# Kernel optimization log

Hardware: AMD Instinct MI355X
Metric: run time of the kernel (lower is better)

The kernel has to match this reference:

```python
import jax, jax.numpy as jnp
import numpy as np
import math

B, T, D = 4, 2048, 1024
NHEAD = 16
HEAD_DIM = D // NHEAD
MAX_REL = 16  # max_relative_position default


def setup_inputs() -> dict:
    key = jax.random.key(0)
    ks = jax.random.split(key, 10)
    s = 1.0 / math.sqrt(D)
    inp = {
        "x": jax.random.normal(ks[0], (B, T, D), dtype=jnp.float32),
        "Wq": jax.random.normal(ks[1], (D, D), dtype=jnp.float32) * s,
        "bq": jnp.zeros((D,), dtype=jnp.float32),
        "Wk": jax.random.normal(ks[2], (D, D), dtype=jnp.float32) * s,
        "bk": jnp.zeros((D,), dtype=jnp.float32),
        "Wv": jax.random.normal(ks[3], (D, D), dtype=jnp.float32) * s,
        "bv": jnp.zeros((D,), dtype=jnp.float32),
        "rel_bias": jax.random.normal(ks[4], (2 * MAX_REL - 1, NHEAD), dtype=jnp.float32) * 0.02,
        "Wo": jax.random.normal(ks[5], (D, D), dtype=jnp.float32) * s,
        "bo": jnp.zeros((D,), dtype=jnp.float32),
    }
    return inp


def _relative_bias(rel_bias, seq_len):
    # distance matrix clamped to [-(MAX_REL-1), MAX_REL-1], shifted to index table
    r = jnp.arange(seq_len)
    dist = jnp.clip(r[None, :] - r[:, None], -MAX_REL + 1, MAX_REL - 1) + MAX_REL - 1
    # gather: [T, T, H] -> [H, T, T]
    return jnp.transpose(rel_bias[dist], (2, 0, 1))


def reference(x, Wq, bq, Wk, bk, Wv, bv, rel_bias, Wo, bo):
    Bdim, Tdim, Ddim = x.shape
    # torch Linear: x @ W.T + b
    Q = x @ Wq.T + bq
    K = x @ Wk.T + bk
    V = x @ Wv.T + bv
    # [B, H, T, hd]
    Q = Q.reshape(Bdim, Tdim, NHEAD, HEAD_DIM).transpose(0, 2, 1, 3)
    K = K.reshape(Bdim, Tdim, NHEAD, HEAD_DIM).transpose(0, 2, 1, 3)
    V = V.reshape(Bdim, Tdim, NHEAD, HEAD_DIM).transpose(0, 2, 1, 3)
    scores = jnp.einsum("bhqd,bhkd->bhqk", Q, K) / math.sqrt(HEAD_DIM)
    scores = scores + _relative_bias(rel_bias, Tdim)[None]  # [1,H,T,T]
    attn = jax.nn.softmax(scores, axis=-1)
    out = jnp.einsum("bhqk,bhkd->bhqd", attn, V)
    out = out.transpose(0, 2, 1, 3).reshape(Bdim, Tdim, Ddim)
    return out @ Wo.T + bo
```

## Files before the change

### kernel.cpp

```cpp
#include <hip/hip_runtime.h>
#include <stdint.h>
#include <math.h>

typedef unsigned short u16;
typedef __bf16 bf16x8 __attribute__((ext_vector_type(8)));
typedef float f32x4 __attribute__((ext_vector_type(4)));
typedef float f32x16 __attribute__((ext_vector_type(16)));
typedef unsigned short u16x8 __attribute__((ext_vector_type(8)));
typedef unsigned short u16x4 __attribute__((ext_vector_type(4)));

#define BATCH 4
#define SEQT 2048
#define DMODEL 1024
#define NHEAD 16
#define HDIM 64
#define LOG2E 1.44269504f

#define LDS_GLD16(gp, lp)                                                     \
  __builtin_amdgcn_global_load_lds(                                           \
      (const __attribute__((address_space(1))) void*)(gp),                    \
      (__attribute__((address_space(3))) void*)(lp), 16, 0, 0)

static __device__ __forceinline__ u16 f2bf(float f) {
  union { float f; uint32_t u; } c; c.f = f;
  uint32_t u = c.u;
  return (u16)((u + 0x7fffu + ((u >> 16) & 1u)) >> 16);
}
static __device__ __forceinline__ u16 f2bf_fast(float f) {
  union { float f; uint32_t u; } c; c.f = f;
  return (u16)((c.u + 0x8000u) >> 16);
}
static __device__ __forceinline__ uint32_t pkbf(float a, float b) {
  union { float f; uint32_t u; } ca, cb; ca.f = a; cb.f = b;
  return __builtin_amdgcn_perm(cb.u + 0x8000u, ca.u + 0x8000u, 0x07060302u);
}
static __device__ __forceinline__ bf16x8 mk_bf8(uint32_t x0, uint32_t x1,
                                                uint32_t x2, uint32_t x3) {
  union { uint32_t u[4]; bf16x8 v; } t;
  t.u[0] = x0; t.u[1] = x1; t.u[2] = x2; t.u[3] = x3;
  return t.v;
}

__global__ __launch_bounds__(256) void k_convert_all(
    const float* __restrict__ x, const float* __restrict__ Wq,
    const float* __restrict__ Wk, const float* __restrict__ Wv,
    const float* __restrict__ Wo, u16* __restrict__ xbf,
    u16* __restrict__ Wqkv, u16* __restrict__ Wob) {
  const int NX4 = 2097152, NW4 = 262144;
  int i = blockIdx.x * 256 + threadIdx.x;
  const float* s; u16* d; int js, jd;
  if (i < NX4) {
    s = x; d = xbf; js = jd = i;
  } else if (i < NX4 + 3 * NW4) {
    int j = i - NX4;
    int w = j >> 18;
    s = (w == 0) ? Wq : (w == 1) ? Wk : Wv;
    js = j & (NW4 - 1);
    d = Wqkv; jd = j;
  } else {
    s = Wo; d = Wob; js = jd = i - NX4 - 3 * NW4;
  }
  float4 v = ((const float4*)s)[js];
  u16x4 o = {f2bf(v.x), f2bf(v.y), f2bf(v.z), f2bf(v.w)};
  ((u16x4*)d)[jd] = o;
}

__global__ __launch_bounds__(256) void k_gemm_qk(
    const u16* __restrict__ A, const u16* __restrict__ Bqk,
    const float* __restrict__ bq_, const float* __restrict__ bk_,
    u16* __restrict__ dq, u16* __restrict__ dk) {
  __shared__ u16 As[128 * 64];
  __shared__ u16 Bs[128 * 64];

  const int tid = threadIdx.x;
  const int wave = tid >> 6, lane = tid & 63;
  const int quad = lane >> 4, l16 = lane & 15;
  const int wm = wave & 1, wn = wave >> 1;
  const int m0 = blockIdx.x * 128, n0 = blockIdx.y * 128;
  const int lrow = lane >> 3, lcol = (lane & 7) * 8;

  f32x4 acc[4][4] = {};

  for (int kt = 0; kt < 1024; kt += 64) {
    __syncthreads();
    for (int c = 0; c < 4; ++c) {
      int rr = (wave * 4 + c) * 8 + lrow;
      LDS_GLD16(A + (size_t)(m0 + rr) * 1024 + kt + lcol,
                &As[(wave * 4 + c) * 512]);
      LDS_GLD16(Bqk + (size_t)(n0 + rr) * 1024 + kt + lcol,
                &Bs[(wave * 4 + c) * 512]);
    }
    __syncthreads();
    for (int kh = 0; kh < 2; ++kh) {
      bf16x8 af[4], bfr[4];
      for (int mt = 0; mt < 4; ++mt)
        af[mt] = *(const bf16x8*)&As[(wm * 64 + mt * 16 + l16) * 64 + kh * 32 +
                                     quad * 8];
      for (int nt = 0; nt < 4; ++nt)
        bfr[nt] = *(const bf16x8*)&Bs[(wn * 64 + nt * 16 + l16) * 64 + kh * 32 +
                                      quad * 8];
      for (int mt = 0; mt < 4; ++mt)
        for (int nt = 0; nt < 4; ++nt)
          acc[mt][nt] = __builtin_amdgcn_mfma_f32_16x16x32_bf16(
              af[mt], bfr[nt], acc[mt][nt], 0, 0, 0);
    }
  }

  u16* dst = (n0 < 1024) ? dq : dk;
  const float* bias = (n0 < 1024) ? bq_ : bk_;
  for (int mt = 0; mt < 4; ++mt)
    for (int nt = 0; nt < 4; ++nt) {
      int nn = (n0 + wn * 64 + nt * 16 + l16) & 1023;
      float bv = bias[nn];
      int h = nn >> 6, hd = nn & 63;
      for (int r = 0; r < 4; ++r) {
        int m = m0 + wm * 64 + mt * 16 + quad * 4 + r;
        int b = m >> 11, t = m & 2047;
        dst[(((size_t)b * NHEAD + h) * SEQT + t) * HDIM + hd] =
            f2bf_fast(acc[mt][nt][r] + bv);
      }
    }
}

__global__ __launch_bounds__(256) void k_gemm_vt(const u16* __restrict__ A,
                                                 const u16* __restrict__ Bx,
                                                 const float* __restrict__ bv_,
                                                 u16* __restrict__ Vt) {
  __shared__ u16 As[128 * 64];
  __shared__ u16 Bs[128 * 64];
  __shared__ float biasS[128];

  const int tid = threadIdx.x;
  const int wave = tid >> 6, lane = tid & 63;
  const int quad = lane >> 4, l16 = lane & 15;
  const int wm = wave & 1, wn = wave >> 1;
  const int m0 = blockIdx.x * 128, n0 = blockIdx.y * 128;
  const int lrow = lane >> 3, lcol = (lane & 7) * 8;

  if (tid < 128) biasS[tid] = bv_[m0 + tid];

  f32x4 acc[4][4] = {};

  for (int kt = 0; kt < 1024; kt += 64) {
    __syncthreads();
    for (int c = 0; c < 4; ++c) {
      int rr = (wave * 4 + c) * 8 + lrow;
      LDS_GLD16(A + (size_t)(m0 + rr) * 1024 + kt + lcol,
                &As[(wave * 4 + c) * 512]);
      LDS_GLD16(Bx + (size_t)(n0 + rr) * 1024 + kt + lcol,
                &Bs[(wave * 4 + c) * 512]);
    }
    __syncthreads();
    for (int kh = 0; kh < 2; ++kh) {
      bf16x8 af[4], bfr[4];
      for (int mt = 0; mt < 4; ++mt)
        af[mt] = *(const bf16x8*)&As[(wm * 64 + mt * 16 + l16) * 64 + kh * 32 +
                                     quad * 8];
      for (int nt = 0; nt < 4; ++nt)
        bfr[nt] = *(const bf16x8*)&Bs[(wn * 64 + nt * 16 + l16) * 64 + kh * 32 +
                                      quad * 8];
      for (int mt = 0; mt < 4; ++mt)
        for (int nt = 0; nt < 4; ++nt)
          acc[mt][nt] = __builtin_amdgcn_mfma_f32_16x16x32_bf16(
              af[mt], bfr[nt], acc[mt][nt], 0, 0, 0);
    }
  }

  for (int mt = 0; mt < 4; ++mt)
    for (int nt = 0; nt < 4; ++nt) {
      int n = n0 + wn * 64 + nt * 16 + l16;
      int b = n >> 11, t = n & 2047;
      for (int r = 0; r < 4; ++r) {
        int m = m0 + wm * 64 + mt * 16 + quad * 4 + r;
        float v = acc[mt][nt][r] + biasS[m - m0];
        Vt[((size_t)(b * NHEAD + (m >> 6)) * HDIM + (m & 63)) * SEQT + t] =
            f2bf_fast(v);
      }
    }
}

__global__ __launch_bounds__(256) void k_gemm_proj(const u16* __restrict__ A,
                                                   const u16* __restrict__ Bm,
                                                   const float* __restrict__ bias,
                                                   float* __restrict__ out) {
  __shared__ u16 As[128 * 64];
  __shared__ u16 Bs[128 * 64];

  const int tid = threadIdx.x;
  const int wave = tid >> 6, lane = tid & 63;
  const int quad = lane >> 4, l16 = lane & 15;
  const int wm = wave & 1, wn = wave >> 1;
  const int m0 = blockIdx.x * 128, n0 = blockIdx.y * 128;
  const int lrow = lane >> 3, lcol = (lane & 7) * 8;

  f32x4 acc[4][4] = {};

  for (int kt = 0; kt < 1024; kt += 64) {
    __syncthreads();
    for (int c = 0; c < 4; ++c) {
      int rr = (wave * 4 + c) * 8 + lrow;
      LDS_GLD16(A + (size_t)(m0 + rr) * 1024 + kt + lcol,
                &As[(wave * 4 + c) * 512]);
      LDS_GLD16(Bm + (size_t)(n0 + rr) * 1024 + kt + lcol,
                &Bs[(wave * 4 + c) * 512]);
    }
    __syncthreads();
    for (int kh = 0; kh < 2; ++kh) {
      bf16x8 af[4], bfr[4];
      for (int mt = 0; mt < 4; ++mt)
        af[mt] = *(const bf16x8*)&As[(wm * 64 + mt * 16 + l16) * 64 + kh * 32 +
                                     quad * 8];
      for (int nt = 0; nt < 4; ++nt)
        bfr[nt] = *(const bf16x8*)&Bs[(wn * 64 + nt * 16 + l16) * 64 + kh * 32 +
                                      quad * 8];
      for (int mt = 0; mt < 4; ++mt)
        for (int nt = 0; nt < 4; ++nt)
          acc[mt][nt] = __builtin_amdgcn_mfma_f32_16x16x32_bf16(
              af[mt], bfr[nt], acc[mt][nt], 0, 0, 0);
    }
  }

  for (int mt = 0; mt < 4; ++mt)
    for (int nt = 0; nt < 4; ++nt) {
      int n = n0 + wn * 64 + nt * 16 + l16;
      float bv = bias[n];
      for (int r = 0; r < 4; ++r) {
        int m = m0 + wm * 64 + mt * 16 + quad * 4 + r;
        out[(size_t)m * 1024 + n] = acc[mt][nt][r] + bv;
      }
    }
}

__global__ __launch_bounds__(256, 4) void k_attn(const u16* __restrict__ Qb,
                                                 const u16* __restrict__ Kb,
                                                 const u16* __restrict__ Vt,
                                                 const float* __restrict__ relb,
                                                 u16* __restrict__ Obf) {
  __shared__ u16 Ks[64 * 64];
  __shared__ u16 VTs[64 * 64];
  __shared__ float biasL[32];

  const int tid = threadIdx.x;
  const int wave = tid >> 6, lane = tid & 63;
  const int l32 = lane & 31, hi = lane >> 5;
  const int qt = blockIdx.x;
  const int bh = blockIdx.y;
  const int h = bh & (NHEAD - 1);
  const size_t base = (size_t)bh * SEQT * HDIM;
  const int qa = qt * 128 + wave * 32;

  if (tid < 31) biasL[tid] = relb[tid * NHEAD + h] * LOG2E;
  const float bLo = relb[0 * NHEAD + h] * LOG2E;
  const float bHi = relb[30 * NHEAD + h] * LOG2E;
  const float CL = 0.125f * LOG2E;

  bf16x8 bq[4];
  {
    const u16* qp = Qb + base + (size_t)(qa + l32) * HDIM + hi * 8;
    for (int ds = 0; ds < 4; ++ds) bq[ds] = *(const bf16x8*)(qp + ds * 16);
  }

  f32x16 Oacc[2] = {};
  float ls = 0.f;

  const int rl = lane >> 3, gb = lane & 7;
  const int row0 = wave * 8 + rl, row1 = row0 + 32;
  const u16* kgp0 = Kb + base + (size_t)row0 * HDIM + ((gb ^ (row0 & 7)) << 3);
  const u16* kgp1 = Kb + base + (size_t)row1 * HDIM + ((gb ^ (row1 & 7)) << 3);
  const u16* vgp0 = Vt + base + (size_t)row0 * SEQT + ((gb ^ (row0 & 7)) << 3);
  const u16* vgp1 = Vt + base + (size_t)row1 * SEQT + ((gb ^ (row1 & 7)) << 3);
  u16* ksl0 = &Ks[wave * 512 + lane * 8];
  u16* ksl1 = ksl0 + 2048;
  u16* vsl0 = &VTs[wave * 512 + lane * 8];
  u16* vsl1 = vsl0 + 2048;

  for (int kt2 = 0; kt2 < 32; ++kt2) {
    const int k0 = kt2 * 64;
    __syncthreads();
    LDS_GLD16(kgp0 + (size_t)k0 * HDIM, ksl0);
    LDS_GLD16(kgp1 + (size_t)k0 * HDIM, ksl1);
    LDS_GLD16(vgp0 + k0, vsl0);
    LDS_GLD16(vgp1 + k0, vsl1);
    __syncthreads();

    for (int kgrp = 0; kgrp < 2; ++kgrp) {
      const int kb = k0 + kgrp * 32;
      f32x16 c = {};
      for (int ds = 0; ds < 4; ++ds) {
        const int key = kgrp * 32 + l32;
        bf16x8 ak = *(const bf16x8*)&Ks[key * 64 +
                                        (((ds * 2 + hi) ^ (key & 7)) << 3)];
        c = __builtin_amdgcn_mfma_f32_32x32x16_bf16(ak, bq[ds], c, 0, 0, 0);
      }

      const int dmin = kb - (qa + 31);
      if (dmin >= 15 || kb + 31 - qa <= -15) {
        const float ub = (dmin >= 15) ? bHi : bLo;
        for (int i = 0; i < 16; ++i)
          c[i] = __builtin_amdgcn_exp2f(fmaf(c[i], CL, ub));
      } else {
        const int dbase = kb + 4 * hi - (qa + l32);
        for (int i = 0; i < 16; ++i) {
          int d = dbase + (i & 3) + 8 * (i >> 2);
          d = d < -15 ? -15 : (d > 15 ? 15 : d);
          c[i] = __builtin_amdgcn_exp2f(fmaf(c[i], CL, biasL[d + 15]));
        }
      }
      {
        float s0 = (c[0] + c[1]) + (c[2] + c[3]);
        float s1 = (c[4] + c[5]) + (c[6] + c[7]);
        float s2 = (c[8] + c[9]) + (c[10] + c[11]);
        float s3 = (c[12] + c[13]) + (c[14] + c[15]);
        ls += (s0 + s1) + (s2 + s3);
      }

      uint32_t p[8];
      for (int i = 0; i < 8; ++i) p[i] = pkbf(c[2 * i], c[2 * i + 1]);

      for (int ks = 0; ks < 2; ++ks) {
        bf16x8 bp = mk_bf8(p[ks * 4 + 0], p[ks * 4 + 1], p[ks * 4 + 2],
                           p[ks * 4 + 3]);
        const int blk = kgrp * 4 + ks * 2;
        for (int dg = 0; dg < 2; ++dg) {
          const int d = dg * 32 + l32;
          const int sw = d & 7;
          uint2 a0 = *(const uint2*)&VTs[d * 64 + ((blk ^ sw) << 3) + 4 * hi];
          uint2 a1 =
              *(const uint2*)&VTs[d * 64 + (((blk + 1) ^ sw) << 3) + 4 * hi];
          bf16x8 av = mk_bf8(a0.x, a0.y, a1.x, a1.y);
          Oacc[dg] = __builtin_amdgcn_mfma_f32_32x32x16_bf16(av, bp, Oacc[dg],
                                                             0, 0, 0);
        }
      }
    }
  }

  ls += __shfl_xor(ls, 32, 64);
  const float rinv = 1.0f / ls;

  const int b = bh >> 4;
  const int t = qa + l32;
  u16* op = Obf + ((size_t)(b * SEQT + t)) * DMODEL + h * HDIM;
  for (int dg = 0; dg < 2; ++dg)
    for (int a = 0; a < 4; ++a) {
      uint2 w;
      w.x = pkbf(Oacc[dg][4 * a + 0] * rinv, Oacc[dg][4 * a + 1] * rinv);
      w.y = pkbf(Oacc[dg][4 * a + 2] * rinv, Oacc[dg][4 * a + 3] * rinv);
      *(uint2*)(op + dg * 32 + 8 * a + 4 * hi) = w;
    }
}

extern "C" void kernel_launch(void* const* d_in, const int* in_sizes, int n_in,
                              void* d_out, int out_size, void* d_ws,
                              size_t ws_size, hipStream_t stream) {
  const float* x = (const float*)d_in[0];
  const float* Wq = (const float*)d_in[1];
  const float* bq = (const float*)d_in[2];
  const float* Wk = (const float*)d_in[3];
  const float* bk = (const float*)d_in[4];
  const float* Wv = (const float*)d_in[5];
  const float* bv = (const float*)d_in[6];
  const float* relb = (const float*)d_in[7];
  const float* Wo = (const float*)d_in[8];
  const float* bo = (const float*)d_in[9];
  float* out = (float*)d_out;

  char* ws = (char*)d_ws;
  const size_t SZ_X = (size_t)BATCH * SEQT * DMODEL * 2;
  const size_t SZ_W = (size_t)DMODEL * DMODEL * 2;
  u16* xbf = (u16*)(ws);
  u16* Wqb = (u16*)(ws + SZ_X);
  u16* Wvb = (u16*)(ws + SZ_X + 2 * SZ_W);
  u16* Wob = (u16*)(ws + SZ_X + 3 * SZ_W);
  u16* Qb = (u16*)(ws + SZ_X + 4 * SZ_W);
  u16* Kb = (u16*)(ws + 2 * SZ_X + 4 * SZ_W);
  u16* Vt = (u16*)(ws + 3 * SZ_X + 4 * SZ_W);
  u16* Obf = (u16*)(ws + 4 * SZ_X + 4 * SZ_W);

  k_convert_all<<<12288, 256, 0, stream>>>(x, Wq, Wk, Wv, Wo, xbf, Wqb, Wob);
  k_gemm_qk<<<dim3(64, 16), 256, 0, stream>>>(xbf, Wqb, bq, bk, Qb, Kb);
  k_gemm_vt<<<dim3(8, 64), 256, 0, stream>>>(Wvb, xbf, bv, Vt);
  k_attn<<<dim3(16, 64), 256, 0, stream>>>(Qb, Kb, Vt, relb, Obf);
  k_gemm_proj<<<dim3(64, 8), 256, 0, stream>>>(Obf, Wob, bo, out);
}
```

Measured before the change: 316.2 us.

## Merge QK and V-transpose GEMMs into one launch and permute Vt for vector LDS reads

```diff
diff --git a/kernel.cpp b/kernel.cpp
--- a/kernel.cpp
+++ b/kernel.cpp
@@ -5,6 +5,7 @@
 typedef unsigned short u16;
 typedef __bf16 bf16x8 __attribute__((ext_vector_type(8)));
 typedef float f32x4 __attribute__((ext_vector_type(4)));
+typedef float f32x2 __attribute__((ext_vector_type(2)));
 typedef float f32x16 __attribute__((ext_vector_type(16)));
 typedef unsigned short u16x8 __attribute__((ext_vector_type(8)));
 typedef unsigned short u16x4 __attribute__((ext_vector_type(4)));
@@ -65,18 +66,29 @@
   ((u16x4*)d)[jd] = o;
 }
 
-__global__ __launch_bounds__(256) void k_gemm_qk(
-    const u16* __restrict__ A, const u16* __restrict__ Bqk,
-    const float* __restrict__ bq_, const float* __restrict__ bk_,
-    u16* __restrict__ dq, u16* __restrict__ dk) {
+__global__ __launch_bounds__(256) void k_gemm_qkvt(
+    const u16* __restrict__ xbf, const u16* __restrict__ Wqk,
+    const u16* __restrict__ Wv, const float* __restrict__ bq_,
+    const float* __restrict__ bk_, const float* __restrict__ bv_,
+    u16* __restrict__ dq, u16* __restrict__ dk, u16* __restrict__ Vt) {
   __shared__ u16 As[128 * 64];
   __shared__ u16 Bs[128 * 64];
+
+  const int bid = blockIdx.x;
+  const bool isQK = bid < 1024;
+  const u16 *Ap, *Bp;
+  int m0, n0;
+  if (isQK) {
+    m0 = (bid & 63) * 128; n0 = (bid >> 6) * 128; Ap = xbf; Bp = Wqk;
+  } else {
+    int j = bid - 1024;
+    m0 = (j & 7) * 128; n0 = (j >> 3) * 128; Ap = Wv; Bp = xbf;
+  }
 
   const int tid = threadIdx.x;
   const int wave = tid >> 6, lane = tid & 63;
   const int quad = lane >> 4, l16 = lane & 15;
   const int wm = wave & 1, wn = wave >> 1;
-  const int m0 = blockIdx.x * 128, n0 = blockIdx.y * 128;
   const int lrow = lane >> 3, lcol = (lane & 7) * 8;
 
   f32x4 acc[4][4] = {};
@@ -85,9 +97,9 @@
     __syncthreads();
     for (int c = 0; c < 4; ++c) {
       int rr = (wave * 4 + c) * 8 + lrow;
-      LDS_GLD16(A + (size_t)(m0 + rr) * 1024 + kt + lcol,
+      LDS_GLD16(Ap + (size_t)(m0 + rr) * 1024 + kt + lcol,
                 &As[(wave * 4 + c) * 512]);
-      LDS_GLD16(Bqk + (size_t)(n0 + rr) * 1024 + kt + lcol,
+      LDS_GLD16(Bp + (size_t)(n0 + rr) * 1024 + kt + lcol,
                 &Bs[(wave * 4 + c) * 512]);
     }
     __syncthreads();
@@ -106,29 +118,43 @@
     }
   }
 
-  u16* dst = (n0 < 1024) ? dq : dk;
-  const float* bias = (n0 < 1024) ? bq_ : bk_;
-  for (int mt = 0; mt < 4; ++mt)
-    for (int nt = 0; nt < 4; ++nt) {
-      int nn = (n0 + wn * 64 + nt * 16 + l16) & 1023;
-      float bv = bias[nn];
-      int h = nn >> 6, hd = nn & 63;
-      for (int r = 0; r < 4; ++r) {
-        int m = m0 + wm * 64 + mt * 16 + quad * 4 + r;
-        int b = m >> 11, t = m & 2047;
-        dst[(((size_t)b * NHEAD + h) * SEQT + t) * HDIM + hd] =
-            f2bf_fast(acc[mt][nt][r] + bv);
-      }
-    }
-}
-
-__global__ __launch_bounds__(256) void k_gemm_vt(const u16* __restrict__ A,
-                                                 const u16* __restrict__ Bx,
-                                                 const float* __restrict__ bv_,
-                                                 u16* __restrict__ Vt) {
+  if (isQK) {
+    u16* dst = (n0 < 1024) ? dq : dk;
+    const float* bias = (n0 < 1024) ? bq_ : bk_;
+    for (int mt = 0; mt < 4; ++mt)
+      for (int nt = 0; nt < 4; ++nt) {
+        int nn = (n0 + wn * 64 + nt * 16 + l16) & 1023;
+        float bv = bias[nn];
+        int h = nn >> 6, hd = nn & 63;
+        for (int r = 0; r < 4; ++r) {
+          int m = m0 + wm * 64 + mt * 16 + quad * 4 + r;
+          int b = m >> 11, t = m & 2047;
+          dst[(((size_t)b * NHEAD + h) * SEQT + t) * HDIM + hd] =
+              f2bf_fast(acc[mt][nt][r] + bv);
+        }
+      }
+  } else {
+    for (int mt = 0; mt < 4; ++mt)
+      for (int nt = 0; nt < 4; ++nt) {
+        int n = n0 + wn * 64 + nt * 16 + l16;
+        int b = n >> 11, t = n & 2047;
+        int tp = (t & ~15) | ((t & 4) << 1) | ((t & 8) >> 1) | (t & 3);
+        for (int r = 0; r < 4; ++r) {
+          int m = m0 + wm * 64 + mt * 16 + quad * 4 + r;
+          float v = acc[mt][nt][r] + bv_[m];
+          Vt[((size_t)(b * NHEAD + (m >> 6)) * HDIM + (m & 63)) * SEQT + tp] =
+              f2bf_fast(v);
+        }
+      }
+  }
+}
+
+__global__ __launch_bounds__(256) void k_gemm_proj(const u16* __restrict__ A,
+                                                   const u16* __restrict__ Bm,
+                                                   const float* __restrict__ bias,
+                                                   float* __restrict__ out) {
   __shared__ u16 As[128 * 64];
   __shared__ u16 Bs[128 * 64];
-  __shared__ float biasS[128];
 
   const int tid = threadIdx.x;
   const int wave = tid >> 6, lane = tid & 63;
@@ -137,8 +163,6 @@
   const int m0 = blockIdx.x * 128, n0 = blockIdx.y * 128;
   const int lrow = lane >> 3, lcol = (lane & 7) * 8;
 
-  if (tid < 128) biasS[tid] = bv_[m0 + tid];
-
   f32x4 acc[4][4] = {};
 
   for (int kt = 0; kt < 1024; kt += 64) {
@@ -147,7 +171,7 @@
       int rr = (wave * 4 + c) * 8 + lrow;
       LDS_GLD16(A + (size_t)(m0 + rr) * 1024 + kt + lcol,
                 &As[(wave * 4 + c) * 512]);
-      LDS_GLD16(Bx + (size_t)(n0 + rr) * 1024 + kt + lcol,
+      LDS_GLD16(Bm + (size_t)(n0 + rr) * 1024 + kt + lcol,
                 &Bs[(wave * 4 + c) * 512]);
     }
     __syncthreads();
@@ -169,60 +193,6 @@
   for (int mt = 0; mt < 4; ++mt)
     for (int nt = 0; nt < 4; ++nt) {
       int n = n0 + wn * 64 + nt * 16 + l16;
-      int b = n >> 11, t = n & 2047;
-      for (int r = 0; r < 4; ++r) {
-        int m = m0 + wm * 64 + mt * 16 + quad * 4 + r;
-        float v = acc[mt][nt][r] + biasS[m - m0];
-        Vt[((size_t)(b * NHEAD + (m >> 6)) * HDIM + (m & 63)) * SEQT + t] =
-            f2bf_fast(v);
-      }
-    }
-}
-
-__global__ __launch_bounds__(256) void k_gemm_proj(const u16* __restrict__ A,
-                                                   const u16* __restrict__ Bm,
-                                                   const float* __restrict__ bias,
-                                                   float* __restrict__ out) {
-  __shared__ u16 As[128 * 64];
-  __shared__ u16 Bs[128 * 64];
-
-  const int tid = threadIdx.x;
-  const int wave = tid >> 6, lane = tid & 63;
-  const int quad = lane >> 4, l16 = lane & 15;
-  const int wm = wave & 1, wn = wave >> 1;
-  const int m0 = blockIdx.x * 128, n0 = blockIdx.y * 128;
-  const int lrow = lane >> 3, lcol = (lane & 7) * 8;
-
-  f32x4 acc[4][4] = {};
-
-  for (int kt = 0; kt < 1024; kt += 64) {
-    __syncthreads();
-    for (int c = 0; c < 4; ++c) {
-      int rr = (wave * 4 + c) * 8 + lrow;
-      LDS_GLD16(A + (size_t)(m0 + rr) * 1024 + kt + lcol,
-                &As[(wave * 4 + c) * 512]);
-      LDS_GLD16(Bm + (size_t)(n0 + rr) * 1024 + kt + lcol,
-                &Bs[(wave * 4 + c) * 512]);
-    }
-    __syncthreads();
-    for (int kh = 0; kh < 2; ++kh) {
-      bf16x8 af[4], bfr[4];
-      for (int mt = 0; mt < 4; ++mt)
-        af[mt] = *(const bf16x8*)&As[(wm * 64 + mt * 16 + l16) * 64 + kh * 32 +
-                                     quad * 8];
-      for (int nt = 0; nt < 4; ++nt)
-        bfr[nt] = *(const bf16x8*)&Bs[(wn * 64 + nt * 16 + l16) * 64 + kh * 32 +
-                                      quad * 8];
-      for (int mt = 0; mt < 4; ++mt)
-        for (int nt = 0; nt < 4; ++nt)
-          acc[mt][nt] = __builtin_amdgcn_mfma_f32_16x16x32_bf16(
-              af[mt], bfr[nt], acc[mt][nt], 0, 0, 0);
-    }
-  }
-
-  for (int mt = 0; mt < 4; ++mt)
-    for (int nt = 0; nt < 4; ++nt) {
-      int n = n0 + wn * 64 + nt * 16 + l16;
       float bv = bias[n];
       for (int r = 0; r < 4; ++r) {
         int m = m0 + wm * 64 + mt * 16 + quad * 4 + r;
@@ -231,11 +201,11 @@
     }
 }
 
-__global__ __launch_bounds__(256, 4) void k_attn(const u16* __restrict__ Qb,
-                                                 const u16* __restrict__ Kb,
-                                                 const u16* __restrict__ Vt,
-                                                 const float* __restrict__ relb,
-                                                 u16* __restrict__ Obf) {
+__global__ __launch_bounds__(256)
+__attribute__((amdgpu_waves_per_eu(4, 4)))
+void k_attn(const u16* __restrict__ Qb, const u16* __restrict__ Kb,
+            const u16* __restrict__ Vt, const float* __restrict__ relb,
+            u16* __restrict__ Obf) {
   __shared__ u16 Ks[64 * 64];
   __shared__ u16 VTs[64 * 64];
   __shared__ float biasL[32];
@@ -261,7 +231,7 @@
   }
 
   f32x16 Oacc[2] = {};
-  float ls = 0.f;
+  f32x2 ls2 = {};
 
   const int rl = lane >> 3, gb = lane & 7;
   const int row0 = wave * 8 + rl, row1 = row0 + 32;
@@ -274,6 +244,23 @@
   u16* vsl0 = &VTs[wave * 512 + lane * 8];
   u16* vsl1 = vsl0 + 2048;
 
+  int akoff[8], avoff[8];
+#pragma unroll
+  for (int kgrp = 0; kgrp < 2; ++kgrp) {
+    const int key = kgrp * 32 + l32;
+#pragma unroll
+    for (int ds = 0; ds < 4; ++ds)
+      akoff[kgrp * 4 + ds] = key * 64 + (((ds * 2 + hi) ^ (key & 7)) << 3);
+#pragma unroll
+    for (int ks = 0; ks < 2; ++ks)
+#pragma unroll
+      for (int dg = 0; dg < 2; ++dg) {
+        const int d = dg * 32 + l32;
+        const int blk = kgrp * 4 + ks * 2 + hi;
+        avoff[(kgrp * 2 + ks) * 2 + dg] = d * 64 + ((blk ^ (d & 7)) << 3);
+      }
+  }
+
   for (int kt2 = 0; kt2 < 32; ++kt2) {
     const int k0 = kt2 * 64;
     __syncthreads();
@@ -283,23 +270,25 @@
     LDS_GLD16(vgp1 + k0, vsl1);
     __syncthreads();
 
+#pragma unroll
     for (int kgrp = 0; kgrp < 2; ++kgrp) {
       const int kb = k0 + kgrp * 32;
       f32x16 c = {};
+#pragma unroll
       for (int ds = 0; ds < 4; ++ds) {
-        const int key = kgrp * 32 + l32;
-        bf16x8 ak = *(const bf16x8*)&Ks[key * 64 +
-                                        (((ds * 2 + hi) ^ (key & 7)) << 3)];
+        bf16x8 ak = *(const bf16x8*)&Ks[akoff[kgrp * 4 + ds]];
         c = __builtin_amdgcn_mfma_f32_32x32x16_bf16(ak, bq[ds], c, 0, 0, 0);
       }
 
       const int dmin = kb - (qa + 31);
       if (dmin >= 15 || kb + 31 - qa <= -15) {
         const float ub = (dmin >= 15) ? bHi : bLo;
+#pragma unroll
         for (int i = 0; i < 16; ++i)
           c[i] = __builtin_amdgcn_exp2f(fmaf(c[i], CL, ub));
       } else {
         const int dbase = kb + 4 * hi - (qa + l32);
+#pragma unroll
         for (int i = 0; i < 16; ++i) {
           int d = dbase + (i & 3) + 8 * (i >> 2);
           d = d < -15 ? -15 : (d > 15 ? 15 : d);
@@ -307,27 +296,24 @@
         }
       }
       {
-        float s0 = (c[0] + c[1]) + (c[2] + c[3]);
-        float s1 = (c[4] + c[5]) + (c[6] + c[7]);
-        float s2 = (c[8] + c[9]) + (c[10] + c[11]);
-        float s3 = (c[12] + c[13]) + (c[14] + c[15]);
-        ls += (s0 + s1) + (s2 + s3);
+        f32x2 s0 = {c[0], c[1]}, s1 = {c[2], c[3]};
+        f32x2 s2 = {c[4], c[5]}, s3 = {c[6], c[7]};
+        f32x2 s4 = {c[8], c[9]}, s5 = {c[10], c[11]};
+        f32x2 s6 = {c[12], c[13]}, s7 = {c[14], c[15]};
+        ls2 += ((s0 + s1) + (s2 + s3)) + ((s4 + s5) + (s6 + s7));
       }
 
       uint32_t p[8];
+#pragma unroll
       for (int i = 0; i < 8; ++i) p[i] = pkbf(c[2 * i], c[2 * i + 1]);
 
+#pragma unroll
       for (int ks = 0; ks < 2; ++ks) {
         bf16x8 bp = mk_bf8(p[ks * 4 + 0], p[ks * 4 + 1], p[ks * 4 + 2],
                            p[ks * 4 + 3]);
-        const int blk = kgrp * 4 + ks * 2;
+#pragma unroll
         for (int dg = 0; dg < 2; ++dg) {
-          const int d = dg * 32 + l32;
-          const int sw = d & 7;
-          uint2 a0 = *(const uint2*)&VTs[d * 64 + ((blk ^ sw) << 3) + 4 * hi];
-          uint2 a1 =
-              *(const uint2*)&VTs[d * 64 + (((blk + 1) ^ sw) << 3) + 4 * hi];
-          bf16x8 av = mk_bf8(a0.x, a0.y, a1.x, a1.y);
+          bf16x8 av = *(const bf16x8*)&VTs[avoff[(kgrp * 2 + ks) * 2 + dg]];
           Oacc[dg] = __builtin_amdgcn_mfma_f32_32x32x16_bf16(av, bp, Oacc[dg],
                                                              0, 0, 0);
         }
@@ -335,13 +321,16 @@
     }
   }
 
+  float ls = ls2.x + ls2.y;
   ls += __shfl_xor(ls, 32, 64);
   const float rinv = 1.0f / ls;
 
   const int b = bh >> 4;
   const int t = qa + l32;
   u16* op = Obf + ((size_t)(b * SEQT + t)) * DMODEL + h * HDIM;
+#pragma unroll
   for (int dg = 0; dg < 2; ++dg)
+#pragma unroll
     for (int a = 0; a < 4; ++a) {
       uint2 w;
       w.x = pkbf(Oacc[dg][4 * a + 0] * rinv, Oacc[dg][4 * a + 1] * rinv);
@@ -378,8 +367,7 @@
   u16* Obf = (u16*)(ws + 4 * SZ_X + 4 * SZ_W);
 
   k_convert_all<<<12288, 256, 0, stream>>>(x, Wq, Wk, Wv, Wo, xbf, Wqb, Wob);
-  k_gemm_qk<<<dim3(64, 16), 256, 0, stream>>>(xbf, Wqb, bq, bk, Qb, Kb);
-  k_gemm_vt<<<dim3(8, 64), 256, 0, stream>>>(Wvb, xbf, bv, Vt);
+  k_gemm_qkvt<<<1536, 256, 0, stream>>>(xbf, Wqb, Wvb, bq, bk, bv, Qb, Kb, Vt);
   k_attn<<<dim3(16, 64), 256, 0, stream>>>(Qb, Kb, Vt, relb, Obf);
   k_gemm_proj<<<dim3(64, 8), 256, 0, stream>>>(Obf, Wob, bo, out);
 }
```

After: 311.9 us. About the same (-1.4%).
